# Kernel optimization log

Hardware: AMD Instinct MI355X
Metric: run time of the kernel (lower is better)

## Reference

```python
import jax, jax.numpy as jnp
import numpy as np

EPS_LN = 1e-5  # torch nn.LayerNorm default

def layernorm(x, g, b):
    mu = x.mean(-1, keepdims=True)
    var = ((x - mu) ** 2).mean(-1, keepdims=True)
    return (x - mu) * jax.lax.rsqrt(var + EPS_LN) * g + b

def softmax_kernel(x, proj, is_query, kernel_eps=1e-4):
    # FAVOR+ positive softmax random features (performer_pytorch math).
    # x: (B,H,N,D) queries/keys, proj: (M,D) random projection.
    d = x.shape[-1]
    norm = d ** -0.25
    ratio = proj.shape[0] ** -0.5
    xd = jnp.einsum('bhnd,md->bhnm', x * norm, proj)
    diag = 0.5 * (x ** 2).sum(-1, keepdims=True) * (norm ** 2)  # (B,H,N,1)
    stab = jnp.max(xd, axis=-1, keepdims=True) if is_query else jnp.max(xd)
    return ratio * (jnp.exp(xd - diag - stab) + kernel_eps)

def linear_attention(q, k, v):
    # Non-causal O(N) attention. q,k: (B,H,N,M); v: (B,H,N,DH)
    k_sum = k.sum(axis=-2)                                      # (B,H,M)
    d_inv = 1.0 / jnp.einsum('bhnm,bhm->bhn', q, k_sum)
    context = jnp.einsum('bhnm,bhnd->bhmd', k, v)               # (B,H,M,DH)
    return jnp.einsum('bhnm,bhmd,bhn->bhnd', q, context, d_inv)

def setup_inputs():
    key = jax.random.key(0)
    B, K, D, H, L = 32, 2048, 256, 4, 2
    DH = D // H
    M = int(DH * np.log(DH))  # 266, performer_pytorch default nb_features
    FF = 4 * D
    ks = jax.random.split(key, 20)
    def w(i, shape):
        return jax.random.normal(ks[i], shape, dtype=jnp.float32) * 0.02
    return dict(
        expr=jax.random.uniform(ks[0], (B, K), dtype=jnp.float32),
        coords=jax.random.uniform(ks[1], (B, 2), dtype=jnp.float32),
        gene_emb=w(2, (K, D)), pos_emb=w(3, (K, D)),
        val_w=w(4, (1, D)), val_b=jnp.zeros((D,), jnp.float32),
        val_ln_g=jnp.ones((D,), jnp.float32), val_ln_b=jnp.zeros((D,), jnp.float32),
        sp_w=w(5, (2, D)), sp_b=jnp.zeros((D,), jnp.float32),
        sp_ln_g=jnp.ones((D,), jnp.float32), sp_ln_b=jnp.zeros((D,), jnp.float32),
        p_ln1_g=jnp.ones((L, D), jnp.float32), p_ln1_b=jnp.zeros((L, D), jnp.float32),
        p_wq=w(6, (L, D, D)), p_bq=jnp.zeros((L, D), jnp.float32),
        p_wk=w(7, (L, D, D)), p_bk=jnp.zeros((L, D), jnp.float32),
        p_wv=w(8, (L, D, D)), p_bv=jnp.zeros((L, D), jnp.float32),
        p_wo=w(9, (L, D, D)), p_bo=jnp.zeros((L, D), jnp.float32),
        p_ln2_g=jnp.ones((L, D), jnp.float32), p_ln2_b=jnp.zeros((L, D), jnp.float32),
        p_ff1_w=w(10, (L, D, FF)), p_ff1_b=jnp.zeros((L, FF), jnp.float32),
        p_ff2_w=w(11, (L, FF, D)), p_ff2_b=jnp.zeros((L, D), jnp.float32),
        proj=jax.random.normal(ks[12], (L, M, DH), dtype=jnp.float32),
        q_w=w(13, (D, D)), q_b=jnp.zeros((D,), jnp.float32),
        k_w=w(14, (D, D)), k_b=jnp.zeros((D,), jnp.float32),
        v_w=w(15, (D, D)), v_b=jnp.zeros((D,), jnp.float32),
        o_w=w(16, (D, D)), o_b=jnp.zeros((D,), jnp.float32),
    )

def reference(expr, coords, gene_emb, pos_emb, val_w, val_b, val_ln_g, val_ln_b,
              sp_w, sp_b, sp_ln_g, sp_ln_b,
              p_ln1_g, p_ln1_b, p_wq, p_bq, p_wk, p_bk, p_wv, p_bv, p_wo, p_bo,
              p_ln2_g, p_ln2_b, p_ff1_w, p_ff1_b, p_ff2_w, p_ff2_b, proj,
              q_w, q_b, k_w, k_b, v_w, v_b, o_w, o_b):
    B, K = expr.shape
    D = gene_emb.shape[1]
    L = p_wq.shape[0]
    H = 4
    DH = D // H
    # gene tokens = gene_id_emb + gene_pos_emb + GELU(LN(Linear(expr)))
    val = jax.nn.gelu(layernorm(expr[..., None] * val_w[0] + val_b, val_ln_g, val_ln_b), approximate=False)
    gene_tokens = (gene_emb + pos_emb)[None] + val                      # (B,K,D)
    sp = jax.nn.gelu(layernorm(coords @ sp_w + sp_b, sp_ln_g, sp_ln_b), approximate=False)
    x = jnp.concatenate([sp[:, None, :], gene_tokens], axis=1)          # (B,K+1,D)
    N = K + 1
    def split_heads(t):
        return t.reshape(B, N, H, DH).transpose(0, 2, 1, 3)
    # Performer: depth x [x + Attn(LN(x)); x + FF(LN(x))], dropout off (eval)
    for l in range(L):
        y = layernorm(x, p_ln1_g[l], p_ln1_b[l])
        q = split_heads(y @ p_wq[l] + p_bq[l])
        k = split_heads(y @ p_wk[l] + p_bk[l])
        v = split_heads(y @ p_wv[l] + p_bv[l])
        qf = softmax_kernel(q, proj[l], True)
        kf = softmax_kernel(k, proj[l], False)
        o = linear_attention(qf, kf, v)                                 # (B,H,N,DH)
        o = o.transpose(0, 2, 1, 3).reshape(B, N, D)
        x = x + (o @ p_wo[l] + p_bo[l])
        y = layernorm(x, p_ln2_g[l], p_ln2_b[l])
        x = x + (jax.nn.gelu(y @ p_ff1_w[l] + p_ff1_b[l], approximate=False) @ p_ff2_w[l] + p_ff2_b[l])
    # single-query cross-attention pooling: spatial token attends to genes
    spatial_out = x[:, :1]
    gene_out = x[:, 1:]
    q = spatial_out @ q_w + q_b                                          # (B,1,D)
    kk = gene_out @ k_w + k_b                                            # (B,K,D)
    vv = gene_out @ v_w + v_b
    attn = jax.nn.softmax(jnp.einsum('bqd,bkd->bqk', q, kk) / (D ** 0.5), axis=-1)
    pooled = jnp.einsum('bqk,bkd->bqd', attn, vv)[:, 0]                  # (B,D)
    return pooled @ o_w + o_b
```

## Files before the change

kernel.cpp:

```cpp
#include <hip/hip_runtime.h>
#include <hip/hip_bf16.h>
#include <math.h>

#define NB   32
#define KG   2048
#define NSEQ 2049
#define DIM  256
#define NH   4
#define DH   64
#define MF   266
#define FFD  1024
#define BN   (NB*NSEQ)
#define FFROWS2 32784
#define NORMC 0.35355339059327376f
#define RATIOC (1.0f/16.309506430300091f)

typedef __attribute__((ext_vector_type(8))) short short8;
typedef __attribute__((ext_vector_type(4))) float f32x4;
#define MFMA16(a,b,c) __builtin_amdgcn_mfma_f32_16x16x32_bf16(a,b,c,0,0,0)

__device__ __forceinline__ short f2b(float f){
  union{ __hip_bfloat16 h; short s;} u; u.h = __float2bfloat16(f); return u.s;
}
__device__ __forceinline__ float b2f(short s){
  union{ short s; __hip_bfloat16 h;} u; u.s = s; return __bfloat162float(u.h);
}
__device__ __forceinline__ float gelu_f(float x){
  return 0.5f*x*(1.0f+erff(x*0.70710678118654752f));
}
__device__ __forceinline__ void gload16(const short* g, short* l){
  __builtin_amdgcn_global_load_lds(
      (const __attribute__((address_space(1))) void*)g,
      (__attribute__((address_space(3))) void*)l, 16, 0, 0);
}
__device__ __forceinline__ float waveSum(float v){
  #pragma unroll
  for(int o=32;o>0;o>>=1) v += __shfl_down(v,o);
  return v;
}
__device__ __forceinline__ float waveMax(float v){
  #pragma unroll
  for(int o=32;o>0;o>>=1) v = fmaxf(v,__shfl_down(v,o));
  return v;
}
__device__ __forceinline__ float xorSum64(float v){
  v += __shfl_xor(v,32); v += __shfl_xor(v,16); v += __shfl_xor(v,8);
  v += __shfl_xor(v,4);  v += __shfl_xor(v,2);  v += __shfl_xor(v,1);
  return v;
}
__device__ __forceinline__ float blockSum256(float v, float* red){
  int lane = threadIdx.x & 63, wid = threadIdx.x >> 6;
  v = waveSum(v);
  __syncthreads();
  if(lane==0) red[wid]=v;
  __syncthreads();
  return red[0]+red[1]+red[2]+red[3];
}
__device__ __forceinline__ float blockMax256(float v, float* red){
  int lane = threadIdx.x & 63, wid = threadIdx.x >> 6;
  v = waveMax(v);
  __syncthreads();
  if(lane==0) red[wid]=v;
  __syncthreads();
  return fmaxf(fmaxf(red[0],red[1]),fmaxf(red[2],red[3]));
}
__device__ __forceinline__ unsigned fenc(float f){
  unsigned u = __float_as_uint(f);
  return (u & 0x80000000u) ? ~u : (u | 0x80000000u);
}
__device__ __forceinline__ float fdec(unsigned u){
  return (u & 0x80000000u) ? __uint_as_float(u & 0x7FFFFFFFu) : __uint_as_float(~u);
}

__global__ __launch_bounds__(256) void embed_kernel(
    const float* __restrict__ expr, const float* __restrict__ coords,
    const float* __restrict__ gene_emb, const float* __restrict__ pos_emb,
    const float* __restrict__ val_w, const float* __restrict__ val_b,
    const float* __restrict__ val_g, const float* __restrict__ val_bb,
    const float* __restrict__ sp_w, const float* __restrict__ sp_b,
    const float* __restrict__ sp_g, const float* __restrict__ sp_bb,
    float* __restrict__ x){
  int w = threadIdx.x >> 6, l = threadIdx.x & 63;
  int row = blockIdx.x*4 + w;
  int b = row / NSEQ, n = row % NSEQ;
  int d0 = l*4;
  float4 v;
  if(n==0){
    float c0 = coords[b*2], c1 = coords[b*2+1];
    float4 w0 = *reinterpret_cast<const float4*>(sp_w + d0);
    float4 w1 = *reinterpret_cast<const float4*>(sp_w + DIM + d0);
    float4 bb = *reinterpret_cast<const float4*>(sp_b + d0);
    v = make_float4(c0*w0.x+c1*w1.x+bb.x, c0*w0.y+c1*w1.y+bb.y,
                    c0*w0.z+c1*w1.z+bb.z, c0*w0.w+c1*w1.w+bb.w);
  } else {
    float e = expr[(size_t)b*KG + (n-1)];
    float4 vw = *reinterpret_cast<const float4*>(val_w + d0);
    float4 vb = *reinterpret_cast<const float4*>(val_b + d0);
    v = make_float4(e*vw.x+vb.x, e*vw.y+vb.y, e*vw.z+vb.z, e*vw.w+vb.w);
  }
  float mu = xorSum64(v.x+v.y+v.z+v.w)*(1.0f/DIM);
  float cx=v.x-mu, cy=v.y-mu, cz=v.z-mu, cw=v.w-mu;
  float var = xorSum64(cx*cx+cy*cy+cz*cz+cw*cw)*(1.0f/DIM);
  float r = rsqrtf(var + 1e-5f);
  float4 g  = (n==0)? *reinterpret_cast<const float4*>(sp_g + d0)
                    : *reinterpret_cast<const float4*>(val_g + d0);
  float4 be = (n==0)? *reinterpret_cast<const float4*>(sp_bb + d0)
                    : *reinterpret_cast<const float4*>(val_bb + d0);
  float4 h = make_float4(gelu_f(cx*r*g.x+be.x), gelu_f(cy*r*g.y+be.y),
                         gelu_f(cz*r*g.z+be.z), gelu_f(cw*r*g.w+be.w));
  if(n!=0){
    float4 ge = *reinterpret_cast<const float4*>(gene_emb + (size_t)(n-1)*DIM + d0);
    float4 pe = *reinterpret_cast<const float4*>(pos_emb  + (size_t)(n-1)*DIM + d0);
    h.x += ge.x+pe.x; h.y += ge.y+pe.y; h.z += ge.z+pe.z; h.w += ge.w+pe.w;
  }
  *reinterpret_cast<float4*>(x + (size_t)row*DIM + d0) = h;
}

__global__ __launch_bounds__(256) void ln_bf4(const float* __restrict__ xin,
    const float* __restrict__ g, const float* __restrict__ bb, short* __restrict__ ybf){
  int w = threadIdx.x >> 6, l = threadIdx.x & 63;
  int row = blockIdx.x*4 + w;
  const float* xr = xin + (size_t)row*DIM;
  float4 v = *reinterpret_cast<const float4*>(xr + l*4);
  float s = xorSum64(v.x+v.y+v.z+v.w);
  float mu = s*(1.0f/DIM);
  float cx=v.x-mu, cy=v.y-mu, cz=v.z-mu, cw=v.w-mu;
  float var = xorSum64(cx*cx+cy*cy+cz*cz+cw*cw)*(1.0f/DIM);
  float r = rsqrtf(var+1e-5f);
  const float4 gv = *reinterpret_cast<const float4*>(g + l*4);
  const float4 bv = *reinterpret_cast<const float4*>(bb + l*4);
  short4 o = make_short4(f2b(cx*r*gv.x+bv.x), f2b(cy*r*gv.y+bv.y),
                         f2b(cz*r*gv.z+bv.z), f2b(cw*r*gv.w+bv.w));
  *reinterpret_cast<short4*>(ybf + (size_t)row*DIM + l*4) = o;
}

__global__ __launch_bounds__(256) void diagk4(const short* __restrict__ kbf, float* __restrict__ diagk){
  int w = threadIdx.x >> 6, l = threadIdx.x & 63;
  int row = blockIdx.x*4 + w;
  int b = row / NSEQ, n = row % NSEQ;
  short4 v = *reinterpret_cast<const short4*>(kbf + (size_t)row*DIM + l*4);
  float a0=b2f(v.x), a1=b2f(v.y), a2=b2f(v.z), a3=b2f(v.w);
  float s = a0*a0+a1*a1+a2*a2+a3*a3;
  s += __shfl_xor(s,1); s += __shfl_xor(s,2);
  s += __shfl_xor(s,4); s += __shfl_xor(s,8);
  if((l&15)==0){
    int h = l>>4;
    diagk[((size_t)(b*NH+h))*NSEQ + n] = 0.0625f*s;
  }
}

#define NW 14
struct WPArgs {
  const float* src[NW];
  short* dst[NW];
  int K[NW], N[NW];
  int ts[NW+1];
};
__global__ __launch_bounds__(256) void wprep_fused(WPArgs a){
  __shared__ float tile[32][33];
  int bx = blockIdx.x, t = threadIdx.x;
  int i = 0;
  while(bx >= a.ts[i+1]) i++;
  int tl = bx - a.ts[i];
  int N = a.N[i], K = a.K[i];
  int tcols = N >> 5;
  int tr = tl / tcols, tc = tl - tr*tcols;
  const float* src = a.src[i];
  short* dst = a.dst[i];
  int r = t>>3, c4 = (t&7)*4;
  float4 v = *reinterpret_cast<const float4*>(src + (size_t)(tr*32+r)*N + tc*32 + c4);
  tile[r][c4+0]=v.x; tile[r][c4+1]=v.y; tile[r][c4+2]=v.z; tile[r][c4+3]=v.w;
  __syncthreads();
  short4 o = make_short4(f2b(tile[c4+0][r]), f2b(tile[c4+1][r]),
                         f2b(tile[c4+2][r]), f2b(tile[c4+3][r]));
  *reinterpret_cast<short4*>(dst + (size_t)(tc*32+r)*K + tr*32 + c4) = o;
}

template<int EPI, int OBF, int WBF>
__global__ __launch_bounds__(256) void mgemm2(
    const short* __restrict__ A, const short* __restrict__ Bt,
    const float* __restrict__ bias, void* __restrict__ Cv,
    int M, int N, int Kd, short* __restrict__ Yb){
  __shared__ short As[128*32];
  __shared__ short Bs[128*32];
  int t=threadIdx.x, l=t&63, w=t>>6, lr=l&15, lk=l>>4;
  int wm=w>>1, wn=w&1;
  int m0=blockIdx.y*128, n0=blockIdx.x*128;
  f32x4 acc[4][4];
  #pragma unroll
  for(int i=0;i<4;i++)
    #pragma unroll
    for(int j=0;j<4;j++) acc[i][j]=f32x4{0.f,0.f,0.f,0.f};
  for(int k0=0;k0<Kd;k0+=32){
    #pragma unroll
    for(int p=0;p<2;p++){
      int chunk = p*256 + t;
      int row = chunk>>2, qc = chunk&3;
      short* lbase = &As[(size_t)(p*256 + w*64)*8];
      gload16(A + (size_t)(m0+row)*Kd + k0 + qc*8, lbase);
    }
    #pragma unroll
    for(int p=0;p<2;p++){
      int chunk = p*256 + t;
      int row = chunk>>2, qc = chunk&3;
      short* lbase = &Bs[(size_t)(p*256 + w*64)*8];
      gload16(Bt + (size_t)(n0+row)*Kd + k0 + qc*8, lbase);
    }
    __syncthreads();
    short8 af[4], bfr[4];
    #pragma unroll
    for(int i=0;i<4;i++) af[i] = *reinterpret_cast<const short8*>(&As[(wm*64+i*16+lr)*32 + lk*8]);
    #pragma unroll
    for(int j=0;j<4;j++) bfr[j] = *reinterpret_cast<const short8*>(&Bs[(wn*64+j*16+lr)*32 + lk*8]);
    #pragma unroll
    for(int i=0;i<4;i++)
      #pragma unroll
      for(int j=0;j<4;j++) acc[i][j] = MFMA16(af[i], bfr[j], acc[i][j]);
    __syncthreads();
  }
  #pragma unroll
  for(int i=0;i<4;i++){
    int gm0 = m0 + wm*64 + i*16 + lk*4;
    #pragma unroll
    for(int j=0;j<4;j++){
      int gc = n0 + wn*64 + j*16 + lr;
      float bs = bias[gc];
      #pragma unroll
      for(int r=0;r<4;r++){
        int gm = gm0 + r;
        if(gm<M){
          float vv = acc[i][j][r] + bs;
          if(EPI==2) vv = gelu_f(vv);
          size_t idx = (size_t)gm*N + gc;
          if(OBF){
            ((short*)Cv)[idx] = f2b(vv);
          } else {
            float* C = (float*)Cv;
            if(EPI==1) vv += C[idx];
            C[idx] = vv;
            if(WBF) Yb[idx] = f2b(vv);
          }
        }
      }
    }
  }
}

__global__ __launch_bounds__(256) void qkv_gemm(
    const short* __restrict__ A, const short* __restrict__ Bt,
    const float* __restrict__ bq, const float* __restrict__ bk, const float* __restrict__ bv,
    short* __restrict__ qd, short* __restrict__ kd, short* __restrict__ vd, int M){
  __shared__ short As[128*32];
  __shared__ short Bs[128*32];
  int t=threadIdx.x, l=t&63, w=t>>6, lr=l&15, lk=l>>4;
  int wm=w>>1, wn=w&1;
  int m0=blockIdx.y*128, n0=blockIdx.x*128;
  f32x4 acc[4][4];
  #pragma unroll
  for(int i=0;i<4;i++)
    #pragma unroll
    for(int j=0;j<4;j++) acc[i][j]=f32x4{0.f,0.f,0.f,0.f};
  for(int k0=0;k0<DIM;k0+=32){
    #pragma unroll
    for(int p=0;p<2;p++){
      int chunk = p*256 + t;
      int row = chunk>>2, qc = chunk&3;
      short* lbase = &As[(size_t)(p*256 + w*64)*8];
      gload16(A + (size_t)(m0+row)*DIM + k0 + qc*8, lbase);
    }
    #pragma unroll
    for(int p=0;p<2;p++){
      int chunk = p*256 + t;
      int row = chunk>>2, qc = chunk&3;
      short* lbase = &Bs[(size_t)(p*256 + w*64)*8];
      gload16(Bt + (size_t)(n0+row)*DIM + k0 + qc*8, lbase);
    }
    __syncthreads();
    short8 af[4], bfr[4];
    #pragma unroll
    for(int i=0;i<4;i++) af[i] = *reinterpret_cast<const short8*>(&As[(wm*64+i*16+lr)*32 + lk*8]);
    #pragma unroll
    for(int j=0;j<4;j++) bfr[j] = *reinterpret_cast<const short8*>(&Bs[(wn*64+j*16+lr)*32 + lk*8]);
    #pragma unroll
    for(int i=0;i<4;i++)
      #pragma unroll
      for(int j=0;j<4;j++) acc[i][j] = MFMA16(af[i], bfr[j], acc[i][j]);
    __syncthreads();
  }
  #pragma unroll
  for(int i=0;i<4;i++){
    int gm0 = m0 + wm*64 + i*16 + lk*4;
    #pragma unroll
    for(int j=0;j<4;j++){
      int gc = n0 + wn*64 + j*16 + lr;
      int sel = gc >> 8, col = gc & 255;
      short* dst = (sel==0)? qd : ((sel==1)? kd : vd);
      const float* bp = (sel==0)? bq : ((sel==1)? bk : bv);
      float bs = bp[col];
      #pragma unroll
      for(int r=0;r<4;r++){
        int gm = gm0 + r;
        if(gm<M) dst[(size_t)gm*DIM + col] = f2b(acc[i][j][r] + bs);
      }
    }
  }
}

__global__ __launch_bounds__(256) void projprep_kernel(const float* __restrict__ proj,
    short* __restrict__ projbf, unsigned* __restrict__ kmax){
  int i = blockIdx.x*256 + threadIdx.x;
  if(i==0) *kmax = 0u;
  if(i < 320*64){
    int m = i>>6, d = i&63;
    float v = (m<MF)? proj[(size_t)m*DH + d]*NORMC : 0.f;
    projbf[i] = f2b(v);
  }
}

__global__ __launch_bounds__(256) void kside_max(
    const short* __restrict__ kbf, const short* __restrict__ projbf,
    unsigned* __restrict__ kmax){
  __shared__ short kS[32*72];
  __shared__ float red[4];
  int t=threadIdx.x, l=t&63, w=t>>6, lr=l&15, lk=l>>4;
  int split = blockIdx.x, bh = blockIdx.y;
  int b=bh>>2, h=bh&3;
  int c0 = split*9, c1 = min(c0+9, 65);
  int nf = (w==3)?5:4;
  short8 apf[5][2];
  #pragma unroll
  for(int fi=0;fi<5;fi++){
    int fr = (fi<4)? (fi*4+w) : 16;
    #pragma unroll
    for(int ks=0;ks<2;ks++)
      apf[fi][ks] = *reinterpret_cast<const short8*>(projbf + (fr*16+lr)*64 + ks*32 + lk*8);
  }
  const short8 z8 = {0,0,0,0,0,0,0,0};
  float lmax = -3.0e38f;
  for(int ch=c0; ch<c1; ++ch){
    int n0 = ch*32;
    __syncthreads();
    {
      int r = t>>3, c8 = (t&7)*8;
      int gn = n0 + r;
      short8 v8 = z8;
      if(gn<NSEQ) v8 = *reinterpret_cast<const short8*>(kbf + ((size_t)(b*NSEQ+gn))*DIM + h*DH + c8);
      *reinterpret_cast<short8*>(&kS[r*72+c8]) = v8;
    }
    __syncthreads();
    for(int fi=0;fi<nf;fi++){
      int fr = (fi<4)? (fi*4+w) : 16;
      #pragma unroll
      for(int fn=0;fn<2;fn++){
        f32x4 xa = f32x4{0.f,0.f,0.f,0.f};
        #pragma unroll
        for(int ks=0;ks<2;ks++){
          short8 bk = *reinterpret_cast<const short8*>(&kS[(fn*16+lr)*72 + ks*32 + lk*8]);
          xa = MFMA16(apf[fi][ks], bk, xa);
        }
        #pragma unroll
        for(int r=0;r<4;r++){
          int m = fr*16 + lk*4 + r;
          int n = n0 + fn*16 + lr;
          if(m<MF && n<NSEQ) lmax = fmaxf(lmax, xa[r]);
        }
      }
    }
  }
  float bm = blockMax256(lmax, red);
  if(t==0) atomicMax(kmax, fenc(bm));
}

__global__ __launch_bounds__(256) void kside_ctx(
    const short* __restrict__ kbf, const short* __restrict__ vbf,
    const short* __restrict__ projbf, const float* __restrict__ diagk,
    const unsigned* __restrict__ kmax, float* __restrict__ ctxP){
  __shared__ short kS[32*72];
  __shared__ short vT[64*40];
  __shared__ short kfS[80*40];
  __shared__ float diagS[32];
  int t=threadIdx.x, l=t&63, w=t>>6, lr=l&15, lk=l>>4;
  int fb=blockIdx.x&3, qh=blockIdx.x>>2, bh=blockIdx.y; int b=bh>>2, h=bh&3;
  int F0 = fb*5;
  int ch0 = qh*33, ch1 = min(65, ch0+33);
  float stab = fdec(*kmax);
  short8 apf0[2], apf1[2];
  #pragma unroll
  for(int ks=0;ks<2;ks++){
    apf0[ks] = *reinterpret_cast<const short8*>(projbf + ((F0+w)*16+lr)*64 + ks*32 + lk*8);
    apf1[ks] = *reinterpret_cast<const short8*>(projbf + ((F0+4)*16+lr)*64 + ks*32 + lk*8);
  }
  f32x4 ctx[5];
  #pragma unroll
  for(int f=0;f<5;f++) ctx[f]=f32x4{0.f,0.f,0.f,0.f};
  f32x4 ksc0 = f32x4{0.f,0.f,0.f,0.f};
  f32x4 ksc1 = f32x4{0.f,0.f,0.f,0.f};
  const short ONE=(short)0x3F80;
  const short8 ones8 = {ONE,ONE,ONE,ONE,ONE,ONE,ONE,ONE};
  const short8 z8 = {0,0,0,0,0,0,0,0};
  for(int ch=ch0; ch<ch1; ++ch){
    int n0 = ch*32;
    __syncthreads();
    {
      int r = t>>3, c8 = (t&7)*8;
      int gn = n0 + r;
      short8 v8 = z8;
      if(gn<NSEQ) v8 = *reinterpret_cast<const short8*>(kbf + ((size_t)(b*NSEQ+gn))*DIM + h*DH + c8);
      *reinterpret_cast<short8*>(&kS[r*72+c8]) = v8;
    }
    #pragma unroll
    for(int p=0;p<4;p++){
      int n2 = 2*w + 8*p;
      int dd = t&63;
      int gn0=n0+n2, gn1=gn0+1;
      short v0 = (gn0<NSEQ)? vbf[((size_t)(b*NSEQ+gn0))*DIM + h*DH + dd] : (short)0;
      short v1 = (gn1<NSEQ)? vbf[((size_t)(b*NSEQ+gn1))*DIM + h*DH + dd] : (short)0;
      *reinterpret_cast<short2*>(&vT[dd*40 + n2]) = make_short2(v0,v1);
    }
    if(t<32) diagS[t] = (n0+t<NSEQ)? diagk[(size_t)bh*NSEQ + n0+t] : 0.f;
    __syncthreads();
    #pragma unroll
    for(int fn=0;fn<2;fn++){
      f32x4 xa = f32x4{0.f,0.f,0.f,0.f};
      #pragma unroll
      for(int ks=0;ks<2;ks++){
        short8 bk = *reinterpret_cast<const short8*>(&kS[(fn*16+lr)*72 + ks*32 + lk*8]);
        xa = MFMA16(apf0[ks], bk, xa);
      }
      float dgn = diagS[fn*16+lr];
      #pragma unroll
      for(int r=0;r<4;r++){
        int m = (F0+w)*16 + lk*4 + r;
        int n = n0 + fn*16 + lr;
        float kf = (m<MF && n<NSEQ)? RATIOC*(__expf(xa[r]-dgn-stab)+1e-4f) : 0.f;
        kfS[(w*16+lk*4+r)*40 + fn*16 + lr] = f2b(kf);
      }
    }
    if(w==0){
      #pragma unroll
      for(int fn=0;fn<2;fn++){
        f32x4 xa = f32x4{0.f,0.f,0.f,0.f};
        #pragma unroll
        for(int ks=0;ks<2;ks++){
          short8 bk = *reinterpret_cast<const short8*>(&kS[(fn*16+lr)*72 + ks*32 + lk*8]);
          xa = MFMA16(apf1[ks], bk, xa);
        }
        float dgn = diagS[fn*16+lr];
        #pragma unroll
        for(int r=0;r<4;r++){
          int m = (F0+4)*16 + lk*4 + r;
          int n = n0 + fn*16 + lr;
          float kf = (m<MF && n<NSEQ)? RATIOC*(__expf(xa[r]-dgn-stab)+1e-4f) : 0.f;
          kfS[(64+lk*4+r)*40 + fn*16 + lr] = f2b(kf);
        }
      }
    }
    __syncthreads();
    short8 bv = *reinterpret_cast<const short8*>(&vT[(w*16+lr)*40 + lk*8]);
    short8 a0 = *reinterpret_cast<const short8*>(&kfS[(w*16+lr)*40 + lk*8]);
    short8 a4 = *reinterpret_cast<const short8*>(&kfS[(64+lr)*40 + lk*8]);
    ksc0 = MFMA16(a0, ones8, ksc0);
    ksc1 = MFMA16(a4, ones8, ksc1);
    #pragma unroll
    for(int fl=0;fl<5;fl++){
      short8 a_ = *reinterpret_cast<const short8*>(&kfS[(fl*16+lr)*40 + lk*8]);
      ctx[fl] = MFMA16(a_, bv, ctx[fl]);
    }
  }
  float* P = ctxP + ((size_t)(qh*128 + bh))*65*320;
  #pragma unroll
  for(int fl=0;fl<5;fl++){
    #pragma unroll
    for(int r=0;r<4;r++){
      int m = (F0+fl)*16 + lk*4 + r;
      P[(size_t)(w*16+lr)*320 + m] = ctx[fl][r];
    }
  }
  if(lr==0){
    #pragma unroll
    for(int r=0;r<4;r++){
      int m = (F0+w)*16 + lk*4 + r;
      P[(size_t)64*320 + m] = ksc0[r];
    }
    if(w==0){
      #pragma unroll
      for(int r=0;r<4;r++){
        int m = (F0+4)*16 + lk*4 + r;
        P[(size_t)64*320 + m] = ksc1[r];
      }
    }
  }
}

__global__ __launch_bounds__(256) void ctx_reduce(const float* __restrict__ ctxP, short* __restrict__ ctxT){
  int row = blockIdx.x, bh = blockIdx.y, t = threadIdx.x;
  short* o = ctxT + ((size_t)bh*80 + row)*288;
  if(row < 65){
    const float* P0 = ctxP + ((size_t)bh*65 + row)*320;
    const float* P1 = ctxP + ((size_t)(128+bh)*65 + row)*320;
    for(int m=t; m<288; m+=256)
      o[m] = (m<272)? f2b(P0[m]+P1[m]) : (short)0;
  } else {
    for(int m=t; m<288; m+=256) o[m] = 0;
  }
}

__global__ __launch_bounds__(256) void qside_mfma(
    const short* __restrict__ qbf, const short* __restrict__ projbf,
    const short* __restrict__ ctxT, short* __restrict__ obf){
  __shared__ short qS[64*72];
  __shared__ short qfS[64*296];
  __shared__ float diagS[64];
  int t=threadIdx.x, l=t&63, w=t>>6, lr=l&15, lk=l>>4;
  int n0 = blockIdx.x*64, bh = blockIdx.y;
  int b = bh>>2, h = bh&3;
  const short8 z8 = {0,0,0,0,0,0,0,0};
  {
    int r = t>>2, c8 = (t&3)*16;
    int gn = n0 + r;
    float ssq = 0.f;
    #pragma unroll
    for(int i=0;i<2;i++){
      short8 v8 = z8;
      if(gn<NSEQ) v8 = *reinterpret_cast<const short8*>(qbf + ((size_t)(b*NSEQ+gn))*DIM + h*DH + c8 + i*8);
      #pragma unroll
      for(int u=0;u<8;u++){ float fv=b2f(v8[u]); ssq += fv*fv; }
      *reinterpret_cast<short8*>(&qS[r*72+c8+i*8]) = v8;
    }
    ssq += __shfl_xor(ssq,1); ssq += __shfl_xor(ssq,2);
    if((t&3)==0) diagS[r] = 0.0625f*ssq;
    #pragma unroll
    for(int i=0;i<4;i++) qfS[r*296 + 272 + (t&3)*4 + i] = 0;
  }
  __syncthreads();
  short8 aq[2];
  #pragma unroll
  for(int ks=0;ks<2;ks++) aq[ks] = *reinterpret_cast<const short8*>(&qS[(w*16+lr)*72 + ks*32 + lk*8]);
  f32x4 acc[17];
  #pragma unroll
  for(int f=0;f<17;f++) acc[f]=f32x4{0.f,0.f,0.f,0.f};
  #pragma unroll
  for(int f=0;f<17;f++){
    #pragma unroll
    for(int ks=0;ks<2;ks++){
      short8 bp = *reinterpret_cast<const short8*>(projbf + (f*16+lr)*64 + ks*32 + lk*8);
      acc[f] = MFMA16(aq[ks], bp, acc[f]);
    }
  }
  float rmax[4];
  #pragma unroll
  for(int r=0;r<4;r++){
    float m = -3.0e38f;
    #pragma unroll
    for(int f=0;f<17;f++){
      float v = (f==16 && lr>=10)? -3.0e38f : acc[f][r];
      m = fmaxf(m,v);
    }
    m = fmaxf(m,__shfl_xor(m,1)); m = fmaxf(m,__shfl_xor(m,2));
    m = fmaxf(m,__shfl_xor(m,4)); m = fmaxf(m,__shfl_xor(m,8));
    rmax[r]=m;
  }
  float dg[4];
  #pragma unroll
  for(int r=0;r<4;r++) dg[r] = diagS[w*16 + lk*4 + r];
  #pragma unroll
  for(int f=0;f<17;f++)
    #pragma unroll
    for(int r=0;r<4;r++){
      float qv = RATIOC*(__expf(acc[f][r] - dg[r] - rmax[r]) + 1e-4f);
      qfS[(w*16+lk*4+r)*296 + f*16 + lr] = f2b(qv);
    }
  __syncthreads();
  f32x4 pv[5];
  #pragma unroll
  for(int f=0;f<5;f++) pv[f]=f32x4{0.f,0.f,0.f,0.f};
  const short* cT = ctxT + (size_t)bh*80*288;
  for(int ks=0;ks<9;ks++){
    short8 a_ = *reinterpret_cast<const short8*>(&qfS[(w*16+lr)*296 + ks*32 + lk*8]);
    #pragma unroll
    for(int f=0;f<5;f++){
      short8 bb = *reinterpret_cast<const short8*>(cT + (f*16+lr)*288 + ks*32 + lk*8);
      pv[f] = MFMA16(a_, bb, pv[f]);
    }
  }
  #pragma unroll
  for(int r=0;r<4;r++){
    int gn = n0 + w*16 + lk*4 + r;
    if(gn>=NSEQ) continue;
    float den = __shfl(pv[4][r], (l & 48), 64);
    float inv = 1.0f/den;
    size_t obase = ((size_t)(b*NSEQ+gn))*DIM + h*DH;
    #pragma unroll
    for(int f=0;f<4;f++) obf[obase + f*16 + lr] = f2b(pv[f][r]*inv);
  }
}

__global__ __launch_bounds__(256) void rowproj_kernel(const float* __restrict__ src,
    const float* __restrict__ W, const float* __restrict__ bias,
    float* __restrict__ dst, int rowstride){
  __shared__ float rs[DIM];
  int b=blockIdx.x, t=threadIdx.x;
  rs[t]=src[(size_t)b*rowstride+t];
  __syncthreads();
  float s=bias[t];
  for(int j=0;j<DIM;j++) s += rs[j]*W[(size_t)j*DIM+t];
  dst[(size_t)b*DIM+t]=s;
}

__global__ __launch_bounds__(256) void pool_scores(const float* __restrict__ qfin,
    const short* __restrict__ kk, float* __restrict__ scb){
  __shared__ float qsh[DIM];
  int kc=blockIdx.x, b=blockIdx.y, t=threadIdx.x;
  qsh[t]=qfin[b*DIM+t];
  __syncthreads();
  int kidx = kc*256 + t;
  const short* kr = kk + ((size_t)(b*NSEQ+1+kidx))*DIM;
  float s=0;
  for(int j8=0;j8<32;j8++){
    short8 kv = *reinterpret_cast<const short8*>(kr + j8*8);
    #pragma unroll
    for(int u=0;u<8;u++) s += qsh[j8*8+u]*b2f(kv[u]);
  }
  scb[(size_t)b*KG + kidx] = s*0.0625f;
}

__global__ __launch_bounds__(256) void pool_pv(const float* __restrict__ scb,
    const short* __restrict__ vv, float* __restrict__ pooled){
  __shared__ float sc[KG];
  __shared__ float red[4];
  int b=blockIdx.x, t=threadIdx.x;
  float ls[8]; float lmax=-3.4e38f;
  #pragma unroll
  for(int i=0;i<8;i++){
    ls[i] = scb[(size_t)b*KG + t + i*256];
    lmax = fmaxf(lmax, ls[i]);
  }
  float gmax=blockMax256(lmax,red);
  float lsum=0;
  #pragma unroll
  for(int i=0;i<8;i++){ float e=__expf(ls[i]-gmax); sc[t+i*256]=e; lsum+=e; }
  float gsum=blockSum256(lsum,red);
  __syncthreads();
  float inv=1.0f/gsum;
  float p=0;
  for(int kidx=0;kidx<KG;kidx++) p += sc[kidx]*b2f(vv[((size_t)(b*NSEQ+1+kidx))*DIM + t]);
  pooled[b*DIM+t]=p*inv;
}

extern "C" void kernel_launch(void* const* d_in, const int* in_sizes, int n_in,
                              void* d_out, int out_size, void* d_ws, size_t ws_size,
                              hipStream_t stream){
  const float* expr   =(const float*)d_in[0];
  const float* coords =(const float*)d_in[1];
  const float* gene_emb=(const float*)d_in[2];
  const float* pos_emb=(const float*)d_in[3];
  const float* val_w  =(const float*)d_in[4];
  const float* val_b  =(const float*)d_in[5];
  const float* val_g  =(const float*)d_in[6];
  const float* val_bb =(const float*)d_in[7];
  const float* sp_w   =(const float*)d_in[8];
  const float* sp_b   =(const float*)d_in[9];
  const float* sp_g   =(const float*)d_in[10];
  const float* sp_bb  =(const float*)d_in[11];
  const float* p_ln1_g=(const float*)d_in[12];
  const float* p_ln1_b=(const float*)d_in[13];
  const float* p_wq   =(const float*)d_in[14];
  const float* p_bq   =(const float*)d_in[15];
  const float* p_wk   =(const float*)d_in[16];
  const float* p_bk   =(const float*)d_in[17];
  const float* p_wv   =(const float*)d_in[18];
  const float* p_bv   =(const float*)d_in[19];
  const float* p_wo   =(const float*)d_in[20];
  const float* p_bo   =(const float*)d_in[21];
  const float* p_ln2_g=(const float*)d_in[22];
  const float* p_ln2_b=(const float*)d_in[23];
  const float* p_ff1_w=(const float*)d_in[24];
  const float* p_ff1_b=(const float*)d_in[25];
  const float* p_ff2_w=(const float*)d_in[26];
  const float* p_ff2_b=(const float*)d_in[27];
  const float* proj   =(const float*)d_in[28];
  const float* q_w    =(const float*)d_in[29];
  const float* q_b    =(const float*)d_in[30];
  const float* k_w    =(const float*)d_in[31];
  const float* k_b    =(const float*)d_in[32];
  const float* v_w    =(const float*)d_in[33];
  const float* v_b    =(const float*)d_in[34];
  const float* o_w    =(const float*)d_in[35];
  const float* o_b    =(const float*)d_in[36];
  float* out = (float*)d_out;

  const size_t BND = (size_t)BN*DIM;
  size_t needB = BND*4 + BND*2*4
               + ((size_t)NB*NH*NSEQ + 4 + 2*(size_t)NB*DIM)*4
               + ((size_t)20480 + 2949120 + 1703936)*2;
  if(ws_size < needB){
    hipMemsetAsync(d_out, 0, (size_t)out_size*sizeof(float), stream);
    return;
  }
  float* ws = (float*)d_ws;
  float* x  = ws;
  short* ybf = (short*)(x + BND);
  short* qbf = ybf + BND;
  short* kbf = qbf + BND;
  short* vbf = kbf + BND;
  float* diagk = (float*)(vbf + BND);
  unsigned* kmax = (unsigned*)(diagk + (size_t)NB*NH*NSEQ);
  float* qfin   = (float*)(kmax+4);
  float* pooled = qfin + NB*DIM;
  short* projbf = (short*)(pooled + NB*DIM);
  short* ctxT   = projbf + 20480;
  short* wt     = ctxT + (size_t)128*80*288;
  const size_t LW = 786432;
  float* ctxP = (float*)ybf;
  float* scb  = diagk;

  {
    WPArgs a;
    short* wtkk = wt + 2*LW;
    short* wtvv = wtkk + 65536;
    const float* s10[10] = {p_wq, p_wk, p_wv, p_wo,
                            p_wq+(size_t)DIM*DIM, p_wk+(size_t)DIM*DIM,
                            p_wv+(size_t)DIM*DIM, p_wo+(size_t)DIM*DIM,
                            k_w, v_w};
    short* d10[10] = {wt, wt+65536, wt+131072, wt+196608,
                      wt+LW, wt+LW+65536, wt+LW+131072, wt+LW+196608,
                      wtkk, wtvv};
    int ti = 0;
    for(int i=0;i<10;i++){
      a.src[i]=s10[i]; a.dst[i]=d10[i]; a.K[i]=DIM; a.N[i]=DIM;
      a.ts[i]=ti; ti+=64;
    }
    const float* sff[4] = {p_ff1_w, p_ff2_w, p_ff1_w+(size_t)DIM*FFD, p_ff2_w+(size_t)FFD*DIM};
    short* dff[4] = {wt+262144, wt+524288, wt+LW+262144, wt+LW+524288};
    int Kff[4] = {DIM, FFD, DIM, FFD};
    int Nff[4] = {FFD, DIM, FFD, DIM};
    for(int i=0;i<4;i++){
      a.src[10+i]=sff[i]; a.dst[10+i]=dff[i]; a.K[10+i]=Kff[i]; a.N[10+i]=Nff[i];
      a.ts[10+i]=ti; ti+=256;
    }
    a.ts[14]=ti;
    wprep_fused<<<1664,256,0,stream>>>(a);
  }

  embed_kernel<<<BN/4,256,0,stream>>>(expr,coords,gene_emb,pos_emb,val_w,val_b,val_g,val_bb,
                                      sp_w,sp_b,sp_g,sp_bb,x);

  dim3 gdd(2, (BN+127)/128);
  dim3 gqkv(6, (BN+127)/128);
  dim3 gff1(8, (FFROWS2+127)/128);
  dim3 gff2(2, (FFROWS2+127)/128);
  dim3 gkm(8, NB*NH);
  dim3 gkc(8, NB*NH);
  dim3 gcr(80, NB*NH);
  dim3 gq((NSEQ+63)/64, NB*NH);
  dim3 gps(8, NB);
  short* wtkk = wt + 2*LW;
  short* wtvv = wtkk + 65536;

  for(int l=0;l<2;l++){
    short* wl = wt + (size_t)l*LW;
    ln_bf4<<<BN/4,256,0,stream>>>(x, p_ln1_g+l*DIM, p_ln1_b+l*DIM, ybf);
    qkv_gemm<<<gqkv,256,0,stream>>>(ybf, wl, p_bq+l*DIM, p_bk+l*DIM, p_bv+l*DIM,
                                    qbf, kbf, vbf, BN);
    diagk4<<<BN/4,256,0,stream>>>(kbf, diagk);
    projprep_kernel<<<80,256,0,stream>>>(proj + (size_t)l*MF*DH, projbf, kmax);
    kside_max<<<gkm,256,0,stream>>>(kbf, projbf, kmax);
    kside_ctx<<<gkc,256,0,stream>>>(kbf, vbf, projbf, diagk, kmax, ctxP);
    ctx_reduce<<<gcr,256,0,stream>>>(ctxP, ctxT);
    qside_mfma<<<gq,256,0,stream>>>(qbf, projbf, ctxT, kbf);
    mgemm2<1,0,0><<<gdd,256,0,stream>>>(kbf, wl+196608, p_bo+l*DIM, x, BN, DIM, DIM, nullptr);
    ln_bf4<<<BN/4,256,0,stream>>>(x, p_ln2_g+l*DIM, p_ln2_b+l*DIM, ybf);
    for(int c2=0;c2<2;c2++){
      size_t roff=(size_t)c2*FFROWS2;
      mgemm2<2,1,0><<<gff1,256,0,stream>>>(ybf+roff*DIM, wl+262144, p_ff1_b+l*FFD, qbf,
                                           FFROWS2, FFD, DIM, nullptr);
      if(l==1)
        mgemm2<1,0,1><<<gff2,256,0,stream>>>(qbf, wl+524288, p_ff2_b+l*DIM, x+roff*DIM,
                                             FFROWS2, DIM, FFD, ybf+roff*DIM);
      else
        mgemm2<1,0,0><<<gff2,256,0,stream>>>(qbf, wl+524288, p_ff2_b+l*DIM, x+roff*DIM,
                                             FFROWS2, DIM, FFD, nullptr);
    }
  }

  mgemm2<0,1,0><<<gdd,256,0,stream>>>(ybf, wtkk, k_b, kbf, BN, DIM, DIM, nullptr);
  mgemm2<0,1,0><<<gdd,256,0,stream>>>(ybf, wtvv, v_b, vbf, BN, DIM, DIM, nullptr);
  rowproj_kernel<<<NB,256,0,stream>>>(x, q_w, q_b, qfin, NSEQ*DIM);
  pool_scores<<<gps,256,0,stream>>>(qfin, kbf, scb);
  pool_pv<<<NB,256,0,stream>>>(scb, vbf, pooled);
  rowproj_kernel<<<NB,256,0,stream>>>(pooled, o_w, o_b, out, DIM);
}
```

Before: 1.663 ms.

## Fuse key diag into QKV GEMM, split kside_ctx three ways, stream q-features

The separate diagk4 kernel is removed, and the per-head squared norm of the keys is computed in the QKV GEMM epilogue from the bf16-rounded outputs. The kside_ctx chunk range is split three ways instead of two (12 blocks in x), and ctx_reduce now sums three partials, which adds parallelism but also partial-buffer traffic. qside_mfma no longer stages the full 17-tile q-feature matrix in shared memory with block barriers. It computes two feature tiles per k-step into a small per-wave scratch buffer, which lowers LDS use and raises occupancy. That path relies on sched_barrier and the wave's own rows instead of __syncthreads.

```diff
diff --git a/kernel.cpp b/kernel.cpp
--- a/kernel.cpp
+++ b/kernel.cpp
@@ -134,21 +134,6 @@
   *reinterpret_cast<short4*>(ybf + (size_t)row*DIM + l*4) = o;
 }
 
-__global__ __launch_bounds__(256) void diagk4(const short* __restrict__ kbf, float* __restrict__ diagk){
-  int w = threadIdx.x >> 6, l = threadIdx.x & 63;
-  int row = blockIdx.x*4 + w;
-  int b = row / NSEQ, n = row % NSEQ;
-  short4 v = *reinterpret_cast<const short4*>(kbf + (size_t)row*DIM + l*4);
-  float a0=b2f(v.x), a1=b2f(v.y), a2=b2f(v.z), a3=b2f(v.w);
-  float s = a0*a0+a1*a1+a2*a2+a3*a3;
-  s += __shfl_xor(s,1); s += __shfl_xor(s,2);
-  s += __shfl_xor(s,4); s += __shfl_xor(s,8);
-  if((l&15)==0){
-    int h = l>>4;
-    diagk[((size_t)(b*NH+h))*NSEQ + n] = 0.0625f*s;
-  }
-}
-
 #define NW 14
 struct WPArgs {
   const float* src[NW];
@@ -249,7 +234,8 @@
 __global__ __launch_bounds__(256) void qkv_gemm(
     const short* __restrict__ A, const short* __restrict__ Bt,
     const float* __restrict__ bq, const float* __restrict__ bk, const float* __restrict__ bv,
-    short* __restrict__ qd, short* __restrict__ kd, short* __restrict__ vd, int M){
+    short* __restrict__ qd, short* __restrict__ kd, short* __restrict__ vd,
+    float* __restrict__ diagk, int M){
   __shared__ short As[128*32];
   __shared__ short Bs[128*32];
   int t=threadIdx.x, l=t&63, w=t>>6, lr=l&15, lk=l>>4;
@@ -287,9 +273,12 @@
       for(int j=0;j<4;j++) acc[i][j] = MFMA16(af[i], bfr[j], acc[i][j]);
     __syncthreads();
   }
+  bool isK = (blockIdx.x==2) || (blockIdx.x==3);
+  int headq = ((n0 + wn*64) - 256) >> 6;
   #pragma unroll
   for(int i=0;i<4;i++){
     int gm0 = m0 + wm*64 + i*16 + lk*4;
+    float sq[4] = {0.f,0.f,0.f,0.f};
     #pragma unroll
     for(int j=0;j<4;j++){
       int gc = n0 + wn*64 + j*16 + lr;
@@ -300,7 +289,26 @@
       #pragma unroll
       for(int r=0;r<4;r++){
         int gm = gm0 + r;
-        if(gm<M) dst[(size_t)gm*DIM + col] = f2b(acc[i][j][r] + bs);
+        if(gm<M){
+          short sv = f2b(acc[i][j][r] + bs);
+          dst[(size_t)gm*DIM + col] = sv;
+          if(isK){ float kv = b2f(sv); sq[r] += kv*kv; }
+        }
+      }
+    }
+    if(isK){
+      #pragma unroll
+      for(int r=0;r<4;r++){
+        float s = sq[r];
+        s += __shfl_xor(s,1); s += __shfl_xor(s,2);
+        s += __shfl_xor(s,4); s += __shfl_xor(s,8);
+        if(lr==0){
+          int gm = gm0 + r;
+          if(gm<M){
+            int bb_ = gm / NSEQ, nn_ = gm - bb_*NSEQ;
+            diagk[((size_t)(bb_*NH+headq))*NSEQ + nn_] = 0.0625f*s;
+          }
+        }
       }
     }
   }
@@ -382,7 +390,7 @@
   int t=threadIdx.x, l=t&63, w=t>>6, lr=l&15, lk=l>>4;
   int fb=blockIdx.x&3, qh=blockIdx.x>>2, bh=blockIdx.y; int b=bh>>2, h=bh&3;
   int F0 = fb*5;
-  int ch0 = qh*33, ch1 = min(65, ch0+33);
+  int ch0 = qh*22, ch1 = min(65, ch0+22);
   float stab = fdec(*kmax);
   short8 apf0[2], apf1[2];
   #pragma unroll
@@ -498,8 +506,9 @@
   if(row < 65){
     const float* P0 = ctxP + ((size_t)bh*65 + row)*320;
     const float* P1 = ctxP + ((size_t)(128+bh)*65 + row)*320;
+    const float* P2 = ctxP + ((size_t)(256+bh)*65 + row)*320;
     for(int m=t; m<288; m+=256)
-      o[m] = (m<272)? f2b(P0[m]+P1[m]) : (short)0;
+      o[m] = (m<272)? f2b(P0[m]+P1[m]+P2[m]) : (short)0;
   } else {
     for(int m=t; m<288; m+=256) o[m] = 0;
   }
@@ -509,7 +518,7 @@
     const short* __restrict__ qbf, const short* __restrict__ projbf,
     const short* __restrict__ ctxT, short* __restrict__ obf){
   __shared__ short qS[64*72];
-  __shared__ short qfS[64*296];
+  __shared__ short sl[64*40];
   __shared__ float diagS[64];
   int t=threadIdx.x, l=t&63, w=t>>6, lr=l&15, lk=l>>4;
   int n0 = blockIdx.x*64, bh = blockIdx.y;
@@ -529,13 +538,14 @@
     }
     ssq += __shfl_xor(ssq,1); ssq += __shfl_xor(ssq,2);
     if((t&3)==0) diagS[r] = 0.0625f*ssq;
-    #pragma unroll
-    for(int i=0;i<4;i++) qfS[r*296 + 272 + (t&3)*4 + i] = 0;
-  }
-  __syncthreads();
+  }
+  __builtin_amdgcn_sched_barrier(0);
   short8 aq[2];
   #pragma unroll
   for(int ks=0;ks<2;ks++) aq[ks] = *reinterpret_cast<const short8*>(&qS[(w*16+lr)*72 + ks*32 + lk*8]);
+  float dg[4];
+  #pragma unroll
+  for(int r=0;r<4;r++) dg[r] = diagS[w*16 + lk*4 + r];
   f32x4 acc[17];
   #pragma unroll
   for(int f=0;f<17;f++) acc[f]=f32x4{0.f,0.f,0.f,0.f};
@@ -560,28 +570,30 @@
     m = fmaxf(m,__shfl_xor(m,4)); m = fmaxf(m,__shfl_xor(m,8));
     rmax[r]=m;
   }
-  float dg[4];
-  #pragma unroll
-  for(int r=0;r<4;r++) dg[r] = diagS[w*16 + lk*4 + r];
-  #pragma unroll
-  for(int f=0;f<17;f++)
-    #pragma unroll
-    for(int r=0;r<4;r++){
-      float qv = RATIOC*(__expf(acc[f][r] - dg[r] - rmax[r]) + 1e-4f);
-      qfS[(w*16+lk*4+r)*296 + f*16 + lr] = f2b(qv);
-    }
-  __syncthreads();
   f32x4 pv[5];
   #pragma unroll
   for(int f=0;f<5;f++) pv[f]=f32x4{0.f,0.f,0.f,0.f};
   const short* cT = ctxT + (size_t)bh*80*288;
+  #pragma unroll
   for(int ks=0;ks<9;ks++){
-    short8 a_ = *reinterpret_cast<const short8*>(&qfS[(w*16+lr)*296 + ks*32 + lk*8]);
-    #pragma unroll
-    for(int f=0;f<5;f++){
-      short8 bb = *reinterpret_cast<const short8*>(cT + (f*16+lr)*288 + ks*32 + lk*8);
-      pv[f] = MFMA16(a_, bb, pv[f]);
-    }
+    #pragma unroll
+    for(int fi=0;fi<2;fi++){
+      int f = ks*2 + fi;
+      #pragma unroll
+      for(int r=0;r<4;r++){
+        float qv = 0.f;
+        if(f<17) qv = RATIOC*(__expf(acc[f][r] - dg[r] - rmax[r]) + 1e-4f);
+        sl[(w*16+lk*4+r)*40 + fi*16 + lr] = f2b(qv);
+      }
+    }
+    __builtin_amdgcn_sched_barrier(0);
+    short8 a_ = *reinterpret_cast<const short8*>(&sl[(w*16+lr)*40 + lk*8]);
+    #pragma unroll
+    for(int f5=0;f5<5;f5++){
+      short8 bb = *reinterpret_cast<const short8*>(cT + (f5*16+lr)*288 + ks*32 + lk*8);
+      pv[f5] = MFMA16(a_, bb, pv[f5]);
+    }
+    __builtin_amdgcn_sched_barrier(0);
   }
   #pragma unroll
   for(int r=0;r<4;r++){
@@ -750,7 +762,7 @@
   dim3 gff1(8, (FFROWS2+127)/128);
   dim3 gff2(2, (FFROWS2+127)/128);
   dim3 gkm(8, NB*NH);
-  dim3 gkc(8, NB*NH);
+  dim3 gkc(12, NB*NH);
   dim3 gcr(80, NB*NH);
   dim3 gq((NSEQ+63)/64, NB*NH);
   dim3 gps(8, NB);
@@ -761,8 +773,7 @@
     short* wl = wt + (size_t)l*LW;
     ln_bf4<<<BN/4,256,0,stream>>>(x, p_ln1_g+l*DIM, p_ln1_b+l*DIM, ybf);
     qkv_gemm<<<gqkv,256,0,stream>>>(ybf, wl, p_bq+l*DIM, p_bk+l*DIM, p_bv+l*DIM,
-                                    qbf, kbf, vbf, BN);
-    diagk4<<<BN/4,256,0,stream>>>(kbf, diagk);
+                                    qbf, kbf, vbf, diagk, BN);
     projprep_kernel<<<80,256,0,stream>>>(proj + (size_t)l*MF*DH, projbf, kmax);
     kside_max<<<gkm,256,0,stream>>>(kbf, projbf, kmax);
     kside_ctx<<<gkc,256,0,stream>>>(kbf, vbf, projbf, diagk, kmax, ctxP);
```

Measured after the change: 1.715 ms. 3.1% more time.
